# Optimization experiments

Measured on AMD Instinct MI355X. Metric: run time of the kernel, lower is better.

## Reference

```python
import jax, jax.numpy as jnp
import numpy as np

D_MODEL = 1024
D_FF = 4096
N_EXPERTS = 8
TOP_K = 2

def setup_inputs() -> dict:
    key = jax.random.key(0)
    ks = jax.random.split(key, 8)
    s = 0.02
    return {
        "x": jax.random.normal(ks[0], (4, 2048, D_MODEL), dtype=jnp.float32),
        "W1": jax.random.normal(ks[1], (N_EXPERTS, D_MODEL, D_FF), dtype=jnp.float32) * s,
        "b1": jnp.zeros((N_EXPERTS, D_FF), dtype=jnp.float32),
        "W2": jax.random.normal(ks[2], (N_EXPERTS, D_FF, D_MODEL), dtype=jnp.float32) * s,
        "b2": jnp.zeros((N_EXPERTS, D_MODEL), dtype=jnp.float32),
        "Wg": jax.random.normal(ks[3], (D_MODEL, N_EXPERTS), dtype=jnp.float32) * s,
        "bg": jnp.zeros((N_EXPERTS,), dtype=jnp.float32),
    }

def reference(x, W1, b1, W2, b2, Wg, bg):
    B, S, D = x.shape
    # Gating network
    gate_logits = jnp.einsum('bsd,de->bse', x, Wg) + bg
    gate_probs = jax.nn.softmax(gate_logits, axis=-1)  # (B,S,E)
    # Top-k routing on softmax probs (matches torch.topk(F.softmax(logits)))
    top_k_probs, top_k_indices = jax.lax.top_k(gate_probs, TOP_K)  # (B,S,k)
    T = B * S
    x_flat = x.reshape(T, D)
    idx_flat = top_k_indices.reshape(T, TOP_K)
    prob_flat = top_k_probs.reshape(T, TOP_K)
    # Per-token combine weight for each expert: sum of top-k probs routed to it
    # combine[t, e] = sum_j prob_flat[t, j] * (idx_flat[t, j] == e)
    onehot = jax.nn.one_hot(idx_flat, N_EXPERTS, dtype=x.dtype)  # (T,k,E)
    combine = jnp.einsum('tk,tke->te', prob_flat, onehot)  # (T,E)
    out = jnp.zeros((T, D), dtype=x.dtype)
    for e in range(N_EXPERTS):  # static small loop over experts
        h = jax.nn.relu(x_flat @ W1[e] + b1[e])  # (T, d_ff)
        y = h @ W2[e] + b2[e]                    # (T, d_model)
        out = out + combine[:, e:e+1] * y
    return out.reshape(B, S, D), gate_probs
```

## Files before the change

### kernel.cpp

```cpp
#include <hip/hip_runtime.h>

#define D_MODEL 1024
#define D_FF    4096
#define N_EXP   8
#define BM 128
#define BN 128
#define BK 32

typedef __attribute__((ext_vector_type(8))) short bf16x8;
typedef __attribute__((ext_vector_type(4))) float f32x4;
typedef unsigned int u32;

__device__ __forceinline__ unsigned short f2bf(float f) {
  union { float f; unsigned u; } v; v.f = f;
  unsigned r = v.u + 0x7FFFu + ((v.u >> 16) & 1u);
  return (unsigned short)(r >> 16);
}

__device__ __forceinline__ void gl_lds16(const void* g, void* l) {
  __builtin_amdgcn_global_load_lds((const __attribute__((address_space(1))) u32*)g,
                                   (__attribute__((address_space(3))) u32*)l, 16, 0, 0);
}

__global__ __launch_bounds__(256)
void transpose_convert_kernel(const float* __restrict__ src, unsigned short* __restrict__ dst,
                              int Ksub, int Nsrc, int k0, int n0, int Nchunk,
                              unsigned long long eStride) {
  __shared__ u32 s32k[32][65];
  int e = blockIdx.z;
  int kb = blockIdx.x * 64, nb = blockIdx.y * 64;
  const float* se = src + (size_t)e * eStride + (size_t)(k0 + kb) * Nsrc + (n0 + nb);
  unsigned short* de = dst + (size_t)e * Nchunk * Ksub + (size_t)nb * Ksub + kb;
  int tid = threadIdx.x;
  int kh = tid >> 4;
  int n4 = (tid & 15) * 4;
  #pragma unroll
  for (int p = 0; p < 2; p++) {
    int k = kh * 2 + p * 32;
    float4 v0 = *(const float4*)(se + (size_t)k * Nsrc + n4);
    float4 v1 = *(const float4*)(se + (size_t)(k + 1) * Nsrc + n4);
    #pragma unroll
    for (int j = 0; j < 4; j++) {
      u32 pk = (u32)f2bf(((const float*)&v0)[j]) |
               ((u32)f2bf(((const float*)&v1)[j]) << 16);
      s32k[k >> 1][n4 + j] = pk;
    }
  }
  __syncthreads();
  #pragma unroll
  for (int c = 0; c < 2; c++) {
    int id = tid + c * 256;
    int n = id >> 3, kc = id & 7;
    uint4 o;
    o.x = s32k[kc * 4 + 0][n];
    o.y = s32k[kc * 4 + 1][n];
    o.z = s32k[kc * 4 + 2][n];
    o.w = s32k[kc * 4 + 3][n];
    *(uint4*)(de + (size_t)n * Ksub + kc * 8) = o;
  }
}

__global__ void gating_kernel(const float* __restrict__ x,
                              const float* __restrict__ Wg,
                              const float* __restrict__ bg,
                              float* __restrict__ gate_out,
                              unsigned short* __restrict__ xb,
                              int* __restrict__ cnt,
                              int* __restrict__ tokIdx,
                              float* __restrict__ tokW, int T) {
  int wv = threadIdx.x >> 6, lane = threadIdx.x & 63;
  int t = blockIdx.x * 4 + wv;
  if (t >= T) return;
  const float* xr = x + (size_t)t * D_MODEL + lane * 16;
  float acc[N_EXP];
  #pragma unroll
  for (int e = 0; e < N_EXP; e++) acc[e] = 0.f;
  ushort4 xc[4];
  #pragma unroll
  for (int q = 0; q < 4; q++) {
    float4 xv = *(const float4*)(xr + q * 4);
    xc[q].x = f2bf(xv.x); xc[q].y = f2bf(xv.y);
    xc[q].z = f2bf(xv.z); xc[q].w = f2bf(xv.w);
    #pragma unroll
    for (int r = 0; r < 4; r++) {
      float xs = ((const float*)&xv)[r];
      const float* wrow = Wg + (size_t)(lane * 16 + q * 4 + r) * N_EXP;
      float4 wa = *(const float4*)wrow;
      float4 wb = *(const float4*)(wrow + 4);
      acc[0] += xs * wa.x; acc[1] += xs * wa.y; acc[2] += xs * wa.z; acc[3] += xs * wa.w;
      acc[4] += xs * wb.x; acc[5] += xs * wb.y; acc[6] += xs * wb.z; acc[7] += xs * wb.w;
    }
  }
  unsigned short* xbr = xb + (size_t)t * D_MODEL + lane * 16;
  #pragma unroll
  for (int q = 0; q < 4; q++) *(ushort4*)(xbr + q * 4) = xc[q];
  #pragma unroll
  for (int off = 32; off > 0; off >>= 1) {
    #pragma unroll
    for (int e = 0; e < N_EXP; e++) acc[e] += __shfl_xor(acc[e], off);
  }
  if (lane == 0) {
    float l[N_EXP], p[N_EXP];
    float m = -1e30f;
    #pragma unroll
    for (int e = 0; e < N_EXP; e++) { l[e] = acc[e] + bg[e]; m = fmaxf(m, l[e]); }
    float s = 0.f;
    #pragma unroll
    for (int e = 0; e < N_EXP; e++) { p[e] = __expf(l[e] - m); s += p[e]; }
    float inv = 1.f / s;
    #pragma unroll
    for (int e = 0; e < N_EXP; e++) { p[e] *= inv; gate_out[(size_t)t * N_EXP + e] = p[e]; }
    int e1 = 0;
    #pragma unroll
    for (int e = 1; e < N_EXP; e++) if (p[e] > p[e1]) e1 = e;
    int e2 = (e1 == 0) ? 1 : 0;
    #pragma unroll
    for (int e = 0; e < N_EXP; e++) if (e != e1 && p[e] > p[e2]) e2 = e;
    int pos = atomicAdd(cnt + e1, 1);
    tokIdx[(size_t)e1 * T + pos] = t; tokW[(size_t)e1 * T + pos] = p[e1];
    pos = atomicAdd(cnt + e2, 1);
    tokIdx[(size_t)e2 * T + pos] = t; tokW[(size_t)e2 * T + pos] = p[e2];
  }
}

__global__ void schedule_kernel(const int* __restrict__ cnt, int* __restrict__ meta,
                                int* __restrict__ tE, int* __restrict__ tB,
                                int* __restrict__ tV, int T, int maxTiles) {
  if (threadIdx.x != 0 || blockIdx.x != 0) return;
  int t = 0;
  for (int e = 0; e < N_EXP; e++) {
    int c = cnt[e];
    for (int r = 0; r < c && t < maxTiles; r += BM) {
      tE[t] = e; tB[t] = e * T + r; tV[t] = min(BM, c - r); t++;
    }
  }
  meta[0] = t;
}

#define STAGE(b, kt) { _Pragma("unroll") for (int p_ = 0; p_ < 2; p_++) { \
    gl_lds16(srcA[p_] + (size_t)(kt) * BK, &LDSU[(b) * 8192 + (w * 32 + p_ * 16) * 32]); \
    gl_lds16(srcB[p_] + (size_t)(kt) * BK, &LDSU[(b) * 8192 + 4096 + (w * 32 + p_ * 16) * 32]); } }

#define COMPUTE(b) { \
    bf16x8 ra[4], rb[4]; \
    _Pragma("unroll") for (int m_ = 0; m_ < 4; m_++) { \
      int row_ = wr * 64 + m_ * 16 + l15; \
      ra[m_] = *(const bf16x8*)&LDSU[(b) * 8192 + row_ * 32 + (((l4 + (row_ >> 1)) & 3) << 3)]; } \
    _Pragma("unroll") for (int n_ = 0; n_ < 4; n_++) { \
      int rb_ = wc * 64 + n_ * 16 + l15; \
      rb[n_] = *(const bf16x8*)&LDSU[(b) * 8192 + 4096 + rb_ * 32 + (((l4 + (rb_ >> 1)) & 3) << 3)]; } \
    _Pragma("unroll") for (int m_ = 0; m_ < 4; m_++) \
      _Pragma("unroll") for (int n_ = 0; n_ < 4; n_++) \
        acc[m_][n_] = __builtin_amdgcn_mfma_f32_16x16x32_bf16(ra[m_], rb[n_], acc[m_][n_], 0, 0, 0); }

#define BAR() { __builtin_amdgcn_s_barrier(); asm volatile("" ::: "memory"); }
#define WAITVM(N) asm volatile("s_waitcnt vmcnt(" #N ")" ::: "memory");

#define PIPELINE(NT) \
  STAGE(0, 0); STAGE(1, 1); \
  for (int kt = 0; kt < (NT) - 2; kt++) { \
    STAGE((kt + 2) % 3, kt + 2); \
    WAITVM(8); BAR(); \
    COMPUTE(kt % 3); \
    BAR(); \
  } \
  WAITVM(4); BAR(); COMPUTE(((NT) - 2) % 3); BAR(); \
  WAITVM(0); BAR(); COMPUTE(((NT) - 1) % 3);

__global__ __launch_bounds__(256)
void gemm1_kernel(const unsigned short* __restrict__ xb,
                  const unsigned short* __restrict__ w1t,
                  const float* __restrict__ b1,
                  const int* __restrict__ meta,
                  const int* __restrict__ tE, const int* __restrict__ tB,
                  const int* __restrict__ tV, const int* __restrict__ tokIdx,
                  unsigned short* __restrict__ h, int FFC, int chunk_off, int ncolLog2) {
  __shared__ unsigned short LDSU[24576];

  int total = gridDim.x;
  int L = blockIdx.x;
  int q = total >> 3, r8 = total & 7;
  int xcd = L & 7, idx = L >> 3;
  int work = (xcd < r8) ? (xcd * (q + 1) + idx) : (r8 * (q + 1) + (xcd - r8) * q + idx);
  int ncol = 1 << ncolLog2;
  int tile = work >> ncolLog2;
  int cb = work & (ncol - 1);
  if (tile >= meta[0]) return;
  int e = tE[tile], base = tB[tile], valid = tV[tile];
  int tid = threadIdx.x;

  int w = tid >> 6, lane = tid & 63;
  int wr = w >> 1, wc = w & 1;
  int l15 = lane & 15, l4 = lane >> 4;
  int lrow = lane >> 2, lch = lane & 3;

  const unsigned short* panel = w1t + (size_t)e * FFC * D_MODEL;
  const unsigned short* srcA[2];
  const unsigned short* srcB[2];
  #pragma unroll
  for (int p = 0; p < 2; p++) {
    int r = w * 32 + p * 16 + lrow;
    int tok = tokIdx[base + (r < valid ? r : valid - 1)];
    int g = (lch - (r >> 1)) & 3;
    srcA[p] = xb + (size_t)tok * D_MODEL + g * 8;
    srcB[p] = panel + (size_t)(cb * BN + r) * D_MODEL + g * 8;
  }

  f32x4 acc[4][4];
  #pragma unroll
  for (int m = 0; m < 4; m++)
    #pragma unroll
    for (int n = 0; n < 4; n++) acc[m][n] = (f32x4){0.f, 0.f, 0.f, 0.f};

  PIPELINE(D_MODEL / BK);

  #pragma unroll
  for (int n = 0; n < 4; n++) {
    int colc = cb * BN + wc * 64 + n * 16 + l15;
    float bias = b1[(size_t)e * D_FF + chunk_off + colc];
    #pragma unroll
    for (int m = 0; m < 4; m++) {
      #pragma unroll
      for (int r = 0; r < 4; r++) {
        int row = wr * 64 + m * 16 + l4 * 4 + r;
        float v = acc[m][n][r] + bias;
        v = v > 0.f ? v : 0.f;
        h[(size_t)(tile * BM + row) * FFC + colc] = f2bf(v);
      }
    }
  }
}

__global__ __launch_bounds__(256)
void gemm2_kernel(const unsigned short* __restrict__ h,
                  const unsigned short* __restrict__ w2t,
                  const float* __restrict__ b2,
                  const int* __restrict__ meta,
                  const int* __restrict__ tE, const int* __restrict__ tB,
                  const int* __restrict__ tV, const int* __restrict__ tokIdx,
                  const float* __restrict__ tokW,
                  float* __restrict__ out, int FFC, int chunk_off) {
  __shared__ unsigned short LDSU[24576];

  int total = gridDim.x;
  int L = blockIdx.x;
  int q = total >> 3, r8 = total & 7;
  int xcd = L & 7, idx = L >> 3;
  int work = (xcd < r8) ? (xcd * (q + 1) + idx) : (r8 * (q + 1) + (xcd - r8) * q + idx);
  int tile = work >> 3;
  int cb = work & 7;
  if (tile >= meta[0]) return;
  int e = tE[tile], base = tB[tile], valid = tV[tile];
  int tid = threadIdx.x;

  int w = tid >> 6, lane = tid & 63;
  int wr = w >> 1, wc = w & 1;
  int l15 = lane & 15, l4 = lane >> 4;
  int lrow = lane >> 2, lch = lane & 3;

  const unsigned short* panel = w2t + (size_t)e * D_MODEL * FFC;
  const unsigned short* srcA[2];
  const unsigned short* srcB[2];
  #pragma unroll
  for (int p = 0; p < 2; p++) {
    int r = w * 32 + p * 16 + lrow;
    int g = (lch - (r >> 1)) & 3;
    srcA[p] = h + (size_t)(tile * BM + r) * FFC + g * 8;
    srcB[p] = panel + (size_t)(cb * BN + r) * FFC + g * 8;
  }

  f32x4 acc[4][4];
  #pragma unroll
  for (int m = 0; m < 4; m++)
    #pragma unroll
    for (int n = 0; n < 4; n++) acc[m][n] = (f32x4){0.f, 0.f, 0.f, 0.f};

  PIPELINE(FFC / BK);

  int addBias = (chunk_off == 0) ? 1 : 0;
  #pragma unroll
  for (int n = 0; n < 4; n++) {
    int colg = cb * BN + wc * 64 + n * 16 + l15;
    float bias = addBias ? b2[(size_t)e * D_MODEL + colg] : 0.f;
    #pragma unroll
    for (int m = 0; m < 4; m++) {
      #pragma unroll
      for (int r = 0; r < 4; r++) {
        int row = wr * 64 + m * 16 + l4 * 4 + r;
        if (row < valid) {
          int tok = tokIdx[base + row];
          float wgt = tokW[base + row];
          float v = (acc[m][n][r] + bias) * wgt;
          atomicAdd(out + (size_t)tok * D_MODEL + colg, v);
        }
      }
    }
  }
}

extern "C" void kernel_launch(void* const* d_in, const int* in_sizes, int n_in,
                              void* d_out, int out_size, void* d_ws, size_t ws_size,
                              hipStream_t stream) {
  const float* x  = (const float*)d_in[0];
  const float* W1 = (const float*)d_in[1];
  const float* b1 = (const float*)d_in[2];
  const float* W2 = (const float*)d_in[3];
  const float* b2 = (const float*)d_in[4];
  const float* Wg = (const float*)d_in[5];
  const float* bg = (const float*)d_in[6];

  int T = in_sizes[0] / D_MODEL;
  float* out = (float*)d_out;
  float* gate_out = out + (size_t)T * D_MODEL;

  char* ws = (char*)d_ws;
  int* cnt  = (int*)(ws + 0);
  int* meta = (int*)(ws + 64);
  int* tE   = (int*)(ws + 128);
  int* tB   = (int*)(ws + 1024);
  int* tV   = (int*)(ws + 2048);
  size_t off = 4096;
  int* tokIdx = (int*)(ws + off);   off += (size_t)N_EXP * T * 4;
  float* tokW = (float*)(ws + off); off += (size_t)N_EXP * T * 4;
  unsigned short* xb = (unsigned short*)(ws + off); off += (size_t)T * D_MODEL * 2;
  off = (off + 255) & ~(size_t)255;

  int maxTiles = (2 * T) / BM + N_EXP;
  int FFC = D_FF;
  while (FFC > 256 &&
         off + (size_t)FFC * (16384 + 16384 + (size_t)maxTiles * BM * 2) > ws_size)
    FFC >>= 1;

  unsigned short* w1t = (unsigned short*)(ws + off); off += (size_t)FFC * 16384;
  unsigned short* w2t = (unsigned short*)(ws + off); off += (size_t)FFC * 16384;
  unsigned short* h   = (unsigned short*)(ws + off);

  hipMemsetAsync(d_out, 0, (size_t)T * D_MODEL * sizeof(float), stream);
  hipMemsetAsync(cnt, 0, N_EXP * sizeof(int), stream);

  gating_kernel<<<(T + 3) / 4, 256, 0, stream>>>(x, Wg, bg, gate_out, xb, cnt, tokIdx, tokW, T);
  schedule_kernel<<<1, 64, 0, stream>>>(cnt, meta, tE, tB, tV, T, maxTiles);

  int ncol1 = FFC / BN;
  int ncol1Log2 = __builtin_ctz(ncol1);
  for (int c = 0; c * FFC < D_FF; c++) {
    transpose_convert_kernel<<<dim3(D_MODEL / 64, FFC / 64, N_EXP), 256, 0, stream>>>(
        W1, w1t, D_MODEL, D_FF, 0, c * FFC, FFC, (unsigned long long)D_MODEL * D_FF);
    transpose_convert_kernel<<<dim3(FFC / 64, D_MODEL / 64, N_EXP), 256, 0, stream>>>(
        W2, w2t, FFC, D_MODEL, c * FFC, 0, D_MODEL, (unsigned long long)D_FF * D_MODEL);
    gemm1_kernel<<<maxTiles * ncol1, 256, 0, stream>>>(
        xb, w1t, b1, meta, tE, tB, tV, tokIdx, h, FFC, c * FFC, ncol1Log2);
    gemm2_kernel<<<maxTiles * (D_MODEL / BN), 256, 0, stream>>>(
        h, w2t, b2, meta, tE, tB, tV, tokIdx, tokW, out, FFC, c * FFC);
  }
}
```

Measured before the change: 776.9 us.

## Drop FF chunking: convert full weights once and run single GEMM passes

Removes the workspace-driven chunk loop over the FF dimension. All expert weights are now converted and transposed up front, followed by one gemm1 and one gemm2 launch over the full D_FF. This cuts launch count and removes the repeated atomic accumulation passes into the output. It also unrolls the 3-stage pipeline so buffer indices are constants, and hoists the bias loads in the gemm2 epilogue. The risk is that the workspace is assumed large enough for the full bf16 weights plus h, with no fallback if it is not.

```diff
diff --git a/kernel.cpp b/kernel.cpp
--- a/kernel.cpp
+++ b/kernel.cpp
@@ -24,13 +24,13 @@
 
 __global__ __launch_bounds__(256)
 void transpose_convert_kernel(const float* __restrict__ src, unsigned short* __restrict__ dst,
-                              int Ksub, int Nsrc, int k0, int n0, int Nchunk,
+                              int Ksub, int Nsrc,
                               unsigned long long eStride) {
   __shared__ u32 s32k[32][65];
   int e = blockIdx.z;
   int kb = blockIdx.x * 64, nb = blockIdx.y * 64;
-  const float* se = src + (size_t)e * eStride + (size_t)(k0 + kb) * Nsrc + (n0 + nb);
-  unsigned short* de = dst + (size_t)e * Nchunk * Ksub + (size_t)nb * Ksub + kb;
+  const float* se = src + (size_t)e * eStride + (size_t)kb * Nsrc + nb;
+  unsigned short* de = dst + (size_t)e * (size_t)Nsrc * Ksub + (size_t)nb * Ksub + kb;
   int tid = threadIdx.x;
   int kh = tid >> 4;
   int n4 = (tid & 15) * 4;
@@ -156,16 +156,16 @@
 #define BAR() { __builtin_amdgcn_s_barrier(); asm volatile("" ::: "memory"); }
 #define WAITVM(N) asm volatile("s_waitcnt vmcnt(" #N ")" ::: "memory");
 
-#define PIPELINE(NT) \
+#define PIPE3(NT) \
   STAGE(0, 0); STAGE(1, 1); \
-  for (int kt = 0; kt < (NT) - 2; kt++) { \
-    STAGE((kt + 2) % 3, kt + 2); \
-    WAITVM(8); BAR(); \
-    COMPUTE(kt % 3); \
-    BAR(); \
+  for (int it = 0; it < ((NT) - 2) / 3; it++) { \
+    int kt = 3 * it; \
+    STAGE(2, kt + 2); WAITVM(8); BAR(); COMPUTE(0); BAR(); \
+    STAGE(0, kt + 3); WAITVM(8); BAR(); COMPUTE(1); BAR(); \
+    STAGE(1, kt + 4); WAITVM(8); BAR(); COMPUTE(2); BAR(); \
   } \
-  WAITVM(4); BAR(); COMPUTE(((NT) - 2) % 3); BAR(); \
-  WAITVM(0); BAR(); COMPUTE(((NT) - 1) % 3);
+  WAITVM(4); BAR(); COMPUTE(0); BAR(); \
+  WAITVM(0); BAR(); COMPUTE(1);
 
 __global__ __launch_bounds__(256)
 void gemm1_kernel(const unsigned short* __restrict__ xb,
@@ -174,7 +174,7 @@
                   const int* __restrict__ meta,
                   const int* __restrict__ tE, const int* __restrict__ tB,
                   const int* __restrict__ tV, const int* __restrict__ tokIdx,
-                  unsigned short* __restrict__ h, int FFC, int chunk_off, int ncolLog2) {
+                  unsigned short* __restrict__ h) {
   __shared__ unsigned short LDSU[24576];
 
   int total = gridDim.x;
@@ -182,9 +182,8 @@
   int q = total >> 3, r8 = total & 7;
   int xcd = L & 7, idx = L >> 3;
   int work = (xcd < r8) ? (xcd * (q + 1) + idx) : (r8 * (q + 1) + (xcd - r8) * q + idx);
-  int ncol = 1 << ncolLog2;
-  int tile = work >> ncolLog2;
-  int cb = work & (ncol - 1);
+  int tile = work >> 5;
+  int cb = work & 31;
   if (tile >= meta[0]) return;
   int e = tE[tile], base = tB[tile], valid = tV[tile];
   int tid = threadIdx.x;
@@ -194,7 +193,7 @@
   int l15 = lane & 15, l4 = lane >> 4;
   int lrow = lane >> 2, lch = lane & 3;
 
-  const unsigned short* panel = w1t + (size_t)e * FFC * D_MODEL;
+  const unsigned short* panel = w1t + (size_t)e * D_FF * D_MODEL;
   const unsigned short* srcA[2];
   const unsigned short* srcB[2];
   #pragma unroll
@@ -212,12 +211,12 @@
     #pragma unroll
     for (int n = 0; n < 4; n++) acc[m][n] = (f32x4){0.f, 0.f, 0.f, 0.f};
 
-  PIPELINE(D_MODEL / BK);
+  PIPE3(D_MODEL / BK);
 
   #pragma unroll
   for (int n = 0; n < 4; n++) {
     int colc = cb * BN + wc * 64 + n * 16 + l15;
-    float bias = b1[(size_t)e * D_FF + chunk_off + colc];
+    float bias = b1[(size_t)e * D_FF + colc];
     #pragma unroll
     for (int m = 0; m < 4; m++) {
       #pragma unroll
@@ -225,7 +224,7 @@
         int row = wr * 64 + m * 16 + l4 * 4 + r;
         float v = acc[m][n][r] + bias;
         v = v > 0.f ? v : 0.f;
-        h[(size_t)(tile * BM + row) * FFC + colc] = f2bf(v);
+        h[(size_t)(tile * BM + row) * D_FF + colc] = f2bf(v);
       }
     }
   }
@@ -239,7 +238,7 @@
                   const int* __restrict__ tE, const int* __restrict__ tB,
                   const int* __restrict__ tV, const int* __restrict__ tokIdx,
                   const float* __restrict__ tokW,
-                  float* __restrict__ out, int FFC, int chunk_off) {
+                  float* __restrict__ out) {
   __shared__ unsigned short LDSU[24576];
 
   int total = gridDim.x;
@@ -258,15 +257,15 @@
   int l15 = lane & 15, l4 = lane >> 4;
   int lrow = lane >> 2, lch = lane & 3;
 
-  const unsigned short* panel = w2t + (size_t)e * D_MODEL * FFC;
+  const unsigned short* panel = w2t + (size_t)e * D_MODEL * D_FF;
   const unsigned short* srcA[2];
   const unsigned short* srcB[2];
   #pragma unroll
   for (int p = 0; p < 2; p++) {
     int r = w * 32 + p * 16 + lrow;
     int g = (lch - (r >> 1)) & 3;
-    srcA[p] = h + (size_t)(tile * BM + r) * FFC + g * 8;
-    srcB[p] = panel + (size_t)(cb * BN + r) * FFC + g * 8;
+    srcA[p] = h + (size_t)(tile * BM + r) * D_FF + g * 8;
+    srcB[p] = panel + (size_t)(cb * BN + r) * D_FF + g * 8;
   }
 
   f32x4 acc[4][4];
@@ -275,24 +274,25 @@
     #pragma unroll
     for (int n = 0; n < 4; n++) acc[m][n] = (f32x4){0.f, 0.f, 0.f, 0.f};
 
-  PIPELINE(FFC / BK);
-
-  int addBias = (chunk_off == 0) ? 1 : 0;
-  #pragma unroll
-  for (int n = 0; n < 4; n++) {
-    int colg = cb * BN + wc * 64 + n * 16 + l15;
-    float bias = addBias ? b2[(size_t)e * D_MODEL + colg] : 0.f;
-    #pragma unroll
-    for (int m = 0; m < 4; m++) {
-      #pragma unroll
-      for (int r = 0; r < 4; r++) {
-        int row = wr * 64 + m * 16 + l4 * 4 + r;
-        if (row < valid) {
-          int tok = tokIdx[base + row];
-          float wgt = tokW[base + row];
-          float v = (acc[m][n][r] + bias) * wgt;
-          atomicAdd(out + (size_t)tok * D_MODEL + colg, v);
-        }
+  PIPE3(D_FF / BK);
+
+  float biasv[4];
+  #pragma unroll
+  for (int n = 0; n < 4; n++)
+    biasv[n] = b2[(size_t)e * D_MODEL + cb * BN + wc * 64 + n * 16 + l15];
+
+  #pragma unroll
+  for (int m = 0; m < 4; m++) {
+    #pragma unroll
+    for (int r = 0; r < 4; r++) {
+      int row = wr * 64 + m * 16 + l4 * 4 + r;
+      if (row < valid) {
+        int tok = tokIdx[base + row];
+        float wgt = tokW[base + row];
+        float* orow = out + (size_t)tok * D_MODEL + cb * BN + wc * 64 + l15;
+        #pragma unroll
+        for (int n = 0; n < 4; n++)
+          atomicAdd(orow + n * 16, (acc[m][n][r] + biasv[n]) * wgt);
       }
     }
   }
@@ -326,13 +326,9 @@
   off = (off + 255) & ~(size_t)255;
 
   int maxTiles = (2 * T) / BM + N_EXP;
-  int FFC = D_FF;
-  while (FFC > 256 &&
-         off + (size_t)FFC * (16384 + 16384 + (size_t)maxTiles * BM * 2) > ws_size)
-    FFC >>= 1;
-
-  unsigned short* w1t = (unsigned short*)(ws + off); off += (size_t)FFC * 16384;
-  unsigned short* w2t = (unsigned short*)(ws + off); off += (size_t)FFC * 16384;
+
+  unsigned short* w1t = (unsigned short*)(ws + off); off += (size_t)N_EXP * D_MODEL * D_FF * 2;
+  unsigned short* w2t = (unsigned short*)(ws + off); off += (size_t)N_EXP * D_MODEL * D_FF * 2;
   unsigned short* h   = (unsigned short*)(ws + off);
 
   hipMemsetAsync(d_out, 0, (size_t)T * D_MODEL * sizeof(float), stream);
@@ -341,16 +337,13 @@
   gating_kernel<<<(T + 3) / 4, 256, 0, stream>>>(x, Wg, bg, gate_out, xb, cnt, tokIdx, tokW, T);
   schedule_kernel<<<1, 64, 0, stream>>>(cnt, meta, tE, tB, tV, T, maxTiles);
 
-  int ncol1 = FFC / BN;
-  int ncol1Log2 = __builtin_ctz(ncol1);
-  for (int c = 0; c * FFC < D_FF; c++) {
-    transpose_convert_kernel<<<dim3(D_MODEL / 64, FFC / 64, N_EXP), 256, 0, stream>>>(
-        W1, w1t, D_MODEL, D_FF, 0, c * FFC, FFC, (unsigned long long)D_MODEL * D_FF);
-    transpose_convert_kernel<<<dim3(FFC / 64, D_MODEL / 64, N_EXP), 256, 0, stream>>>(
-        W2, w2t, FFC, D_MODEL, c * FFC, 0, D_MODEL, (unsigned long long)D_FF * D_MODEL);
-    gemm1_kernel<<<maxTiles * ncol1, 256, 0, stream>>>(
-        xb, w1t, b1, meta, tE, tB, tV, tokIdx, h, FFC, c * FFC, ncol1Log2);
-    gemm2_kernel<<<maxTiles * (D_MODEL / BN), 256, 0, stream>>>(
-        h, w2t, b2, meta, tE, tB, tV, tokIdx, tokW, out, FFC, c * FFC);
-  }
-}
+  transpose_convert_kernel<<<dim3(D_MODEL / 64, D_FF / 64, N_EXP), 256, 0, stream>>>(
+      W1, w1t, D_MODEL, D_FF, (unsigned long long)D_MODEL * D_FF);
+  transpose_convert_kernel<<<dim3(D_FF / 64, D_MODEL / 64, N_EXP), 256, 0, stream>>>(
+      W2, w2t, D_FF, D_MODEL, (unsigned long long)D_FF * D_MODEL);
+
+  gemm1_kernel<<<maxTiles * (D_FF / BN), 256, 0, stream>>>(
+      xb, w1t, b1, meta, tE, tB, tV, tokIdx, h);
+  gemm2_kernel<<<maxTiles * (D_MODEL / BN), 256, 0, stream>>>(
+      h, w2t, b2, meta, tE, tB, tV, tokIdx, tokW, out);
+}
```

Result: faster. 739.5 us (-4.8%).
